# Optimization experiments

Hardware: AMD Instinct MI355X
Metric: run time of the kernel (lower is better)

Reference implementation:

```python
import jax, jax.numpy as jnp
import numpy as np

DEPTH, FEAT, HID = 20, 2048, 1024
HALF = FEAT // 2
CLAMP = 2.0
TWO_OVER_PI = 0.6366197723675814  # FrEIA's 0.636619772


def setup_inputs() -> dict:
    key = jax.random.key(0)
    ks = jax.random.split(key, 9)
    x = jax.random.normal(ks[0], (4096, FEAT), dtype=jnp.float32)
    # FrEIA PermuteRandom: numpy permutation seeded with layer index k
    perms = jnp.asarray(
        np.stack([np.random.RandomState(k).permutation(FEAT) for k in range(DEPTH)]),
        dtype=jnp.int32,
    )
    def w(k, shape):  # module reinits all params as 0.01*randn
        return 0.01 * jax.random.normal(k, shape, dtype=jnp.float32)
    return {
        "x": x, "perms": perms,
        "s1_w1": w(ks[1], (DEPTH, HALF, HID)), "s1_b1": w(ks[2], (DEPTH, HID)),
        "s1_w2": w(ks[3], (DEPTH, HID, FEAT)), "s1_b2": w(ks[4], (DEPTH, FEAT)),
        "s2_w1": w(ks[5], (DEPTH, HALF, HID)), "s2_b1": w(ks[6], (DEPTH, HID)),
        "s2_w2": w(ks[7], (DEPTH, HID, FEAT)), "s2_b2": w(ks[8], (DEPTH, FEAT)),
    }


def _subnet(x, w1, b1, w2, b2):
    h = x @ w1 + b1
    h = jnp.where(h >= 0, h, 0.01 * h)  # LeakyReLU(negative_slope=0.01)
    return h @ w2 + b2


def reference(x, perms, s1_w1, s1_b1, s1_w2, s1_b2, s2_w1, s2_b1, s2_w2, s2_b2):
    def body(carry, xs):
        z, jac = carry
        perm, w1a, b1a, w1b, b1b, w2a, b2a, w2b, b2b = xs
        z = z[:, perm]                       # PermuteRandom
        x1, x2 = z[:, :HALF], z[:, HALF:]    # GLOW coupling split
        r2 = _subnet(x2, w2a, b2a, w2b, b2b)  # [B, FEAT] -> (s2, t2)
        e2 = CLAMP * TWO_OVER_PI * jnp.arctan(r2[:, :HALF] / CLAMP)
        y1 = jnp.exp(e2) * x1 + r2[:, HALF:]
        r1 = _subnet(y1, w1a, b1a, w1b, b1b)  # (s1, t1)
        e1 = CLAMP * TWO_OVER_PI * jnp.arctan(r1[:, :HALF] / CLAMP)
        y2 = jnp.exp(e1) * x2 + r1[:, HALF:]
        jac = jac + e1.sum(-1) + e2.sum(-1)  # log|det J| per sample
        return (jnp.concatenate([y1, y2], axis=-1), jac), None

    jac0 = jnp.zeros(x.shape[0], dtype=x.dtype)
    (z, jac), _ = jax.lax.scan(
        body, (x, jac0),
        (perms, s1_w1, s1_b1, s1_w2, s1_b2, s2_w1, s2_b1, s2_w2, s2_b2),
    )
    return z, jac
```

## Files before the change

### kernel.cpp

```cpp
#include <hip/hip_runtime.h>
#include <stdint.h>

#define DEPTH 20
#define FEAT  2048
#define HALF  1024
#define HID   1024
#define MROWS 4096

typedef __bf16 bf16x8 __attribute__((ext_vector_type(8)));
typedef float  f32x4  __attribute__((ext_vector_type(4)));
typedef unsigned int u32x4 __attribute__((ext_vector_type(4)));

__device__ __forceinline__ unsigned short f2bf(float f) {
  union { float f; unsigned int u; } v; v.f = f;
  unsigned int u = v.u + 0x7fffu + ((v.u >> 16) & 1u);
  return (unsigned short)(u >> 16);
}

__device__ __forceinline__ void async_cp16(unsigned short* lds, const unsigned short* g) {
  __builtin_amdgcn_global_load_lds(
      (const __attribute__((address_space(1))) void*)g,
      (__attribute__((address_space(3))) void*)lds, 16, 0, 0);
}

__device__ __forceinline__ bf16x8 lds_ld8(const unsigned short* p) {
  return __builtin_bit_cast(bf16x8, *(const u32x4*)p);
}

__device__ __forceinline__ void wg_barrier() {
  asm volatile("" ::: "memory");
  __builtin_amdgcn_s_barrier();
  asm volatile("" ::: "memory");
}

__global__ void wcvt_k(const float* __restrict__ s2w1, const float* __restrict__ s2w2,
                       const float* __restrict__ s1w1, const float* __restrict__ s1w2,
                       unsigned short* __restrict__ w2a, unsigned short* __restrict__ w2b,
                       unsigned short* __restrict__ w1a, unsigned short* __restrict__ w1b) {
  const int zid = blockIdx.z;
  const int d = zid >> 2, which = zid & 3;
  const float* src; unsigned short* dst; int N, pp;
  switch (which) {
    case 0:  src = s2w1 + (size_t)d * HALF * HID;  dst = w2a + (size_t)d * HALF * HID; N = 1024; pp = 0; break;
    case 1:  src = s2w2 + (size_t)d * HID * FEAT;  dst = w2b + (size_t)d * FEAT * HID; N = 2048; pp = 1; break;
    case 2:  src = s1w1 + (size_t)d * HALF * HID;  dst = w1a + (size_t)d * HALF * HID; N = 1024; pp = 0; break;
    default: src = s1w2 + (size_t)d * HID * FEAT;  dst = w1b + (size_t)d * FEAT * HID; N = 2048; pp = 1; break;
  }
  int nb = blockIdx.x * 32;
  if (nb >= N) return;
  int kb = blockIdx.y * 32;
  __shared__ float t[32][33];
  int tx = threadIdx.x, ty = threadIdx.y;
#pragma unroll
  for (int s = 0; s < 4; ++s)
    t[ty + 8*s][tx] = src[(size_t)(kb + ty + 8*s) * N + nb + tx];
  __syncthreads();
  int pbase = pp ? (nb < 1024 ? 2*nb : 2*(nb - 1024) + 32) : nb;
#pragma unroll
  for (int s = 0; s < 4; ++s) {
    int nl = ty + 8*s;
    dst[(size_t)(pbase + nl) * 1024 + kb + tx] = f2bf(t[tx][nl]);
  }
}

__device__ __forceinline__ int porig(int p) {
  int g = p >> 6, o = p & 63;
  return (o < 32) ? (g*32 + o) : (1024 + g*32 + (o - 32));
}

__global__ void bias_k(const float* __restrict__ s2b1, const float* __restrict__ s2b2,
                       const float* __restrict__ s1b1, const float* __restrict__ s1b2,
                       float* __restrict__ b2a, float* __restrict__ b2b,
                       float* __restrict__ b1a, float* __restrict__ b1b) {
  int i = blockIdx.x * 256 + threadIdx.x;
  if (i >= DEPTH * 6144) return;
  int d = i / 6144, j = i - d * 6144;
  if (j < 1024)      b2a[d*1024 + j] = s2b1[(size_t)d*HID + j];
  else if (j < 3072) { int p = j - 1024; b2b[d*2048 + p] = s2b2[(size_t)d*FEAT + porig(p)]; }
  else if (j < 4096) b1a[d*1024 + j - 3072] = s1b1[(size_t)d*HID + j - 3072];
  else               { int p = j - 4096; b1b[d*2048 + p] = s1b2[(size_t)d*FEAT + porig(p)]; }
}

__global__ void permute_k(const float* __restrict__ z, const int* __restrict__ perm,
                          float* __restrict__ x1f, float* __restrict__ x2f,
                          unsigned short* __restrict__ x2b) {
  int c = blockIdx.x * 256 + threadIdx.x;
  int row0 = blockIdx.y * 8;
  int pc = perm[c];
#pragma unroll
  for (int r = 0; r < 8; ++r) {
    int row = row0 + r;
    float v = z[row * FEAT + pc];
    if (c < HALF) {
      x1f[row * HALF + c] = v;
    } else {
      x2f[row * HALF + c - HALF] = v;
      x2b[row * HALF + c - HALF] = f2bf(v);
    }
  }
}

template<int EPI>
__launch_bounds__(256)
__global__ void gemm_k(const unsigned short* __restrict__ A,
                       const unsigned short* __restrict__ Bt,
                       const float* __restrict__ bias,
                       const float* __restrict__ xin,
                       float* __restrict__ yout,
                       unsigned short* __restrict__ ybf,
                       float* __restrict__ jac,
                       unsigned short* __restrict__ hout) {
  __shared__ unsigned short As[3][128 * 32];
  __shared__ unsigned short Bs[3][128 * 32];
  const int tid  = threadIdx.x;
  const int wave = tid >> 6, lane = tid & 63;
  const int quad = lane >> 4, l15 = lane & 15;
  const int wy = wave >> 1, wx = wave & 1;
  const int bm = blockIdx.y * 128;
  const int bn = blockIdx.x * 128;
  const int K = 1024;

  f32x4 acc[4][4];
#pragma unroll
  for (int i = 0; i < 4; ++i)
#pragma unroll
    for (int j = 0; j < 4; ++j)
#pragma unroll
      for (int r = 0; r < 4; ++r) acc[i][j][r] = 0.0f;

  const int gbase = wave * 64 + lane;

  auto stage = [&](int kt, int buf) {
    const int k0 = kt * 32;
#pragma unroll
    for (int i = 0; i < 2; ++i) {
      int g  = i * 256 + gbase;
      int r  = g >> 2, kg = g & 3;
      async_cp16(&As[buf][(i * 256 + wave * 64) * 8], A  + (size_t)(bm + r) * K + k0 + kg * 8);
      async_cp16(&Bs[buf][(i * 256 + wave * 64) * 8], Bt + (size_t)(bn + r) * K + k0 + kg * 8);
    }
  };

  stage(0, 0);
  stage(1, 1);

  int cb = 0;
  for (int kt = 0; kt < 32; ++kt) {
    if (kt < 30) {
      stage(kt + 2, (kt + 2) % 3);
      asm volatile("s_waitcnt vmcnt(8)" ::: "memory");
    } else if (kt == 30) {
      asm volatile("s_waitcnt vmcnt(4)" ::: "memory");
    } else {
      asm volatile("s_waitcnt vmcnt(0)" ::: "memory");
    }
    wg_barrier();

    bf16x8 af[4], bf[4];
#pragma unroll
    for (int i = 0; i < 4; ++i)
      af[i] = lds_ld8(&As[cb][(wy * 64 + i * 16 + l15) * 32 + quad * 8]);
#pragma unroll
    for (int j = 0; j < 4; ++j)
      bf[j] = lds_ld8(&Bs[cb][(wx * 64 + j * 16 + l15) * 32 + quad * 8]);
#pragma unroll
    for (int i = 0; i < 4; ++i)
#pragma unroll
      for (int j = 0; j < 4; ++j)
        acc[i][j] = __builtin_amdgcn_mfma_f32_16x16x32_bf16(af[i], bf[j], acc[i][j], 0, 0, 0);

    wg_barrier();
    cb = (cb == 2) ? 0 : cb + 1;
  }

  if (EPI == 0) {
    const int ldo = gridDim.x * 128;
#pragma unroll
    for (int j = 0; j < 4; ++j) {
      int col = bn + wx * 64 + j * 16 + l15;
      float bj = bias[col];
#pragma unroll
      for (int i = 0; i < 4; ++i) {
#pragma unroll
        for (int r = 0; r < 4; ++r) {
          int row = bm + wy * 64 + i * 16 + quad * 4 + r;
          float v = acc[i][j][r] + bj;
          v = v >= 0.0f ? v : 0.01f * v;
          hout[(size_t)row * ldo + col] = f2bf(v);
        }
      }
    }
  } else {
    const int g = (bn >> 6) + wx;
#pragma unroll
    for (int i = 0; i < 4; ++i) {
      float esum[4] = {0.0f, 0.0f, 0.0f, 0.0f};
#pragma unroll
      for (int j = 0; j < 2; ++j) {
        int pe = bn + wx * 64 + j * 16 + l15;
        float be = bias[pe];
        float ba = bias[pe + 32];
        int xcol = g * 32 + j * 16 + l15;
#pragma unroll
        for (int r = 0; r < 4; ++r) {
          int row = bm + wy * 64 + i * 16 + quad * 4 + r;
          float re = acc[i][j][r] + be;
          float ra = acc[i][j + 2][r] + ba;
          float e  = 1.2732395447351628f * atanf(0.5f * re);
          float y  = __expf(e) * xin[(size_t)row * HALF + xcol] + ra;
          yout[(size_t)row * FEAT + xcol] = y;
          if (ybf) ybf[(size_t)row * HALF + xcol] = f2bf(y);
          esum[r] += e;
        }
      }
#pragma unroll
      for (int r = 0; r < 4; ++r) {
        float v = esum[r];
        v += __shfl_xor(v, 1);
        v += __shfl_xor(v, 2);
        v += __shfl_xor(v, 4);
        v += __shfl_xor(v, 8);
        if (l15 == 0) {
          int row = bm + wy * 64 + i * 16 + quad * 4 + r;
          atomicAdd(&jac[row], v);
        }
      }
    }
  }
}

__global__ void jcopy_k(const float* __restrict__ jac, float* __restrict__ out) {
  int i = blockIdx.x * 256 + threadIdx.x;
  if (i < 4096) out[i] = jac[i];
}

extern "C" void kernel_launch(void* const* d_in, const int* in_sizes, int n_in,
                              void* d_out, int out_size, void* d_ws, size_t ws_size,
                              hipStream_t stream) {
  const float* x     = (const float*)d_in[0];
  const int*   perms = (const int*)d_in[1];
  const float* s1w1  = (const float*)d_in[2];
  const float* s1b1  = (const float*)d_in[3];
  const float* s1w2  = (const float*)d_in[4];
  const float* s1b2  = (const float*)d_in[5];
  const float* s2w1  = (const float*)d_in[6];
  const float* s2b1  = (const float*)d_in[7];
  const float* s2w2  = (const float*)d_in[8];
  const float* s2b2  = (const float*)d_in[9];
  float* out = (float*)d_out;

  size_t off = 0;
  char* base = (char*)d_ws;
  auto alloc = [&](size_t bytes) {
    void* r = base + off;
    off += (bytes + 255) & ~(size_t)255;
    return r;
  };
  float*          x1f = (float*)alloc((size_t)MROWS * HALF * 4);
  float*          x2f = (float*)alloc((size_t)MROWS * HALF * 4);
  unsigned short* x2b = (unsigned short*)alloc((size_t)MROWS * HALF * 2);
  unsigned short* y1b = (unsigned short*)alloc((size_t)MROWS * HALF * 2);
  unsigned short* hb  = (unsigned short*)alloc((size_t)MROWS * HID * 2);
  float*          zbuf= (float*)alloc((size_t)MROWS * FEAT * 4);
  unsigned short* w2a = (unsigned short*)alloc((size_t)DEPTH * HALF * HID * 2);
  unsigned short* w2b = (unsigned short*)alloc((size_t)DEPTH * FEAT * HID * 2);
  unsigned short* w1a = (unsigned short*)alloc((size_t)DEPTH * HALF * HID * 2);
  unsigned short* w1b = (unsigned short*)alloc((size_t)DEPTH * FEAT * HID * 2);
  float* b2a = (float*)alloc((size_t)DEPTH * 1024 * 4);
  float* b2b = (float*)alloc((size_t)DEPTH * 2048 * 4);
  float* b1a = (float*)alloc((size_t)DEPTH * 1024 * 4);
  float* b1b = (float*)alloc((size_t)DEPTH * 2048 * 4);
  float* jac = (float*)alloc(4096 * 4);

  hipMemsetAsync(jac, 0, 4096 * 4, stream);

  wcvt_k<<<dim3(64, 32, 4 * DEPTH), dim3(32, 8), 0, stream>>>(
      s2w1, s2w2, s1w1, s1w2, w2a, w2b, w1a, w1b);
  bias_k<<<(DEPTH * 6144 + 255) / 256, 256, 0, stream>>>(
      s2b1, s2b2, s1b1, s1b2, b2a, b2b, b1a, b1b);

  for (int d = 0; d < DEPTH; ++d) {
    const float* zsrc = (d == 0) ? x : zbuf;
    permute_k<<<dim3(8, 512), 256, 0, stream>>>(zsrc, perms + (size_t)d * FEAT, x1f, x2f, x2b);

    unsigned short* W2a = w2a + (size_t)d * HALF * HID;
    unsigned short* W2b = w2b + (size_t)d * FEAT * HID;
    unsigned short* W1a = w1a + (size_t)d * HALF * HID;
    unsigned short* W1b = w1b + (size_t)d * FEAT * HID;
    float* B2a = b2a + (size_t)d * 1024;
    float* B2b = b2b + (size_t)d * 2048;
    float* B1a = b1a + (size_t)d * 1024;
    float* B1b = b1b + (size_t)d * 2048;

    float* zdst = (d == DEPTH - 1) ? out : zbuf;
    gemm_k<0><<<dim3(8, 32), 256, 0, stream>>>(x2b, W2a, B2a, nullptr, nullptr, nullptr, nullptr, hb);
    gemm_k<1><<<dim3(16, 32), 256, 0, stream>>>(hb, W2b, B2b, x1f, zdst, y1b, jac, nullptr);
    gemm_k<0><<<dim3(8, 32), 256, 0, stream>>>(y1b, W1a, B1a, nullptr, nullptr, nullptr, nullptr, hb);
    gemm_k<1><<<dim3(16, 32), 256, 0, stream>>>(hb, W1b, B1b, x2f, zdst + HALF, nullptr, jac, nullptr);
  }
  jcopy_k<<<16, 256, 0, stream>>>(jac, out + (size_t)MROWS * FEAT);
}
```

Before: 4.081 ms.

## Fuse next-layer permutation into coupling epilogue and simplify GEMM pipeline

Precomputes inverse permutations and has the coupling GEMM epilogue scatter outputs directly into the next layer's permuted x1/x2/bf16 buffers (ping-ponged), eliminating the per-layer permute kernel and the z round trip. The GEMM loses its triple-buffered async prefetch in favor of a single buffer with full waits, and the hidden-layer GEMMs use 64-row tiles for more blocks. The weight conversion kernel processes taller tiles with paired bf16 stores. Scattered epilogue writes are less coalesced, and the unpipelined main loop exposes memory latency.

```diff
diff --git a/kernel.cpp b/kernel.cpp
--- a/kernel.cpp
+++ b/kernel.cpp
@@ -25,12 +25,6 @@
 
 __device__ __forceinline__ bf16x8 lds_ld8(const unsigned short* p) {
   return __builtin_bit_cast(bf16x8, *(const u32x4*)p);
-}
-
-__device__ __forceinline__ void wg_barrier() {
-  asm volatile("" ::: "memory");
-  __builtin_amdgcn_s_barrier();
-  asm volatile("" ::: "memory");
 }
 
 __global__ void wcvt_k(const float* __restrict__ s2w1, const float* __restrict__ s2w2,
@@ -48,18 +42,21 @@
   }
   int nb = blockIdx.x * 32;
   if (nb >= N) return;
-  int kb = blockIdx.y * 32;
-  __shared__ float t[32][33];
+  int kb = blockIdx.y * 64;
+  __shared__ float t[64][33];
   int tx = threadIdx.x, ty = threadIdx.y;
 #pragma unroll
-  for (int s = 0; s < 4; ++s)
+  for (int s = 0; s < 8; ++s)
     t[ty + 8*s][tx] = src[(size_t)(kb + ty + 8*s) * N + nb + tx];
   __syncthreads();
   int pbase = pp ? (nb < 1024 ? 2*nb : 2*(nb - 1024) + 32) : nb;
 #pragma unroll
   for (int s = 0; s < 4; ++s) {
     int nl = ty + 8*s;
-    dst[(size_t)(pbase + nl) * 1024 + kb + tx] = f2bf(t[tx][nl]);
+    ushort2 w;
+    w.x = f2bf(t[2*tx][nl]);
+    w.y = f2bf(t[2*tx + 1][nl]);
+    *(ushort2*)&dst[(size_t)(pbase + nl) * 1024 + kb + 2*tx] = w;
   }
 }
 
@@ -81,6 +78,13 @@
   else               { int p = j - 4096; b1b[d*2048 + p] = s1b2[(size_t)d*FEAT + porig(p)]; }
 }
 
+__global__ void invp_k(const int* __restrict__ perms, int* __restrict__ invp) {
+  int i = blockIdx.x * 256 + threadIdx.x;
+  if (i >= DEPTH * FEAT) return;
+  int d = i >> 11, c = i & 2047;
+  invp[(d << 11) | perms[i]] = c;
+}
+
 __global__ void permute_k(const float* __restrict__ z, const int* __restrict__ perm,
                           float* __restrict__ x1f, float* __restrict__ x2f,
                           unsigned short* __restrict__ x2b) {
@@ -106,23 +110,31 @@
                        const unsigned short* __restrict__ Bt,
                        const float* __restrict__ bias,
                        const float* __restrict__ xin,
-                       float* __restrict__ yout,
+                       const int* __restrict__ invp,
+                       float* __restrict__ nx1,
+                       float* __restrict__ nx2,
+                       unsigned short* __restrict__ nx2b,
+                       float* __restrict__ outz,
+                       int zbase,
                        unsigned short* __restrict__ ybf,
                        float* __restrict__ jac,
                        unsigned short* __restrict__ hout) {
-  __shared__ unsigned short As[3][128 * 32];
-  __shared__ unsigned short Bs[3][128 * 32];
+  constexpr int BM = EPI ? 128 : 64;
+  constexpr int MI = EPI ? 4 : 2;
+  constexpr int WR = EPI ? 64 : 32;
+  __shared__ unsigned short As[BM * 32];
+  __shared__ unsigned short Bs[128 * 32];
   const int tid  = threadIdx.x;
   const int wave = tid >> 6, lane = tid & 63;
   const int quad = lane >> 4, l15 = lane & 15;
   const int wy = wave >> 1, wx = wave & 1;
-  const int bm = blockIdx.y * 128;
+  const int bm = blockIdx.y * BM;
   const int bn = blockIdx.x * 128;
   const int K = 1024;
 
-  f32x4 acc[4][4];
-#pragma unroll
-  for (int i = 0; i < 4; ++i)
+  f32x4 acc[MI][4];
+#pragma unroll
+  for (int i = 0; i < MI; ++i)
 #pragma unroll
     for (int j = 0; j < 4; ++j)
 #pragma unroll
@@ -130,47 +142,36 @@
 
   const int gbase = wave * 64 + lane;
 
-  auto stage = [&](int kt, int buf) {
+  for (int kt = 0; kt < 32; ++kt) {
     const int k0 = kt * 32;
+#pragma unroll
+    for (int i = 0; i < BM / 64; ++i) {
+      int g  = i * 256 + gbase;
+      int r  = g >> 2, kg = g & 3;
+      async_cp16(&As[(i * 256 + wave * 64) * 8], A  + (size_t)(bm + r) * K + k0 + kg * 8);
+    }
 #pragma unroll
     for (int i = 0; i < 2; ++i) {
       int g  = i * 256 + gbase;
       int r  = g >> 2, kg = g & 3;
-      async_cp16(&As[buf][(i * 256 + wave * 64) * 8], A  + (size_t)(bm + r) * K + k0 + kg * 8);
-      async_cp16(&Bs[buf][(i * 256 + wave * 64) * 8], Bt + (size_t)(bn + r) * K + k0 + kg * 8);
-    }
-  };
-
-  stage(0, 0);
-  stage(1, 1);
-
-  int cb = 0;
-  for (int kt = 0; kt < 32; ++kt) {
-    if (kt < 30) {
-      stage(kt + 2, (kt + 2) % 3);
-      asm volatile("s_waitcnt vmcnt(8)" ::: "memory");
-    } else if (kt == 30) {
-      asm volatile("s_waitcnt vmcnt(4)" ::: "memory");
-    } else {
-      asm volatile("s_waitcnt vmcnt(0)" ::: "memory");
-    }
-    wg_barrier();
-
-    bf16x8 af[4], bf[4];
-#pragma unroll
-    for (int i = 0; i < 4; ++i)
-      af[i] = lds_ld8(&As[cb][(wy * 64 + i * 16 + l15) * 32 + quad * 8]);
+      async_cp16(&Bs[(i * 256 + wave * 64) * 8], Bt + (size_t)(bn + r) * K + k0 + kg * 8);
+    }
+    asm volatile("s_waitcnt vmcnt(0)" ::: "memory");
+    __syncthreads();
+
+    bf16x8 af[MI], bf[4];
+#pragma unroll
+    for (int i = 0; i < MI; ++i)
+      af[i] = lds_ld8(&As[(wy * WR + i * 16 + l15) * 32 + quad * 8]);
 #pragma unroll
     for (int j = 0; j < 4; ++j)
-      bf[j] = lds_ld8(&Bs[cb][(wx * 64 + j * 16 + l15) * 32 + quad * 8]);
-#pragma unroll
-    for (int i = 0; i < 4; ++i)
+      bf[j] = lds_ld8(&Bs[(wx * 64 + j * 16 + l15) * 32 + quad * 8]);
+#pragma unroll
+    for (int i = 0; i < MI; ++i)
 #pragma unroll
       for (int j = 0; j < 4; ++j)
         acc[i][j] = __builtin_amdgcn_mfma_f32_16x16x32_bf16(af[i], bf[j], acc[i][j], 0, 0, 0);
-
-    wg_barrier();
-    cb = (cb == 2) ? 0 : cb + 1;
+    __syncthreads();
   }
 
   if (EPI == 0) {
@@ -180,10 +181,10 @@
       int col = bn + wx * 64 + j * 16 + l15;
       float bj = bias[col];
 #pragma unroll
-      for (int i = 0; i < 4; ++i) {
+      for (int i = 0; i < MI; ++i) {
 #pragma unroll
         for (int r = 0; r < 4; ++r) {
-          int row = bm + wy * 64 + i * 16 + quad * 4 + r;
+          int row = bm + wy * WR + i * 16 + quad * 4 + r;
           float v = acc[i][j][r] + bj;
           v = v >= 0.0f ? v : 0.01f * v;
           hout[(size_t)row * ldo + col] = f2bf(v);
@@ -192,24 +193,38 @@
     }
   } else {
     const int g = (bn >> 6) + wx;
+    float be[2], ba[2];
+    int xcol[2], route[2];
+#pragma unroll
+    for (int j = 0; j < 2; ++j) {
+      int pe = bn + wx * 64 + j * 16 + l15;
+      be[j] = bias[pe];
+      ba[j] = bias[pe + 32];
+      xcol[j] = g * 32 + j * 16 + l15;
+      int zcol = zbase + xcol[j];
+      route[j] = invp ? invp[zcol] : zcol;
+    }
 #pragma unroll
     for (int i = 0; i < 4; ++i) {
       float esum[4] = {0.0f, 0.0f, 0.0f, 0.0f};
 #pragma unroll
       for (int j = 0; j < 2; ++j) {
-        int pe = bn + wx * 64 + j * 16 + l15;
-        float be = bias[pe];
-        float ba = bias[pe + 32];
-        int xcol = g * 32 + j * 16 + l15;
 #pragma unroll
         for (int r = 0; r < 4; ++r) {
           int row = bm + wy * 64 + i * 16 + quad * 4 + r;
-          float re = acc[i][j][r] + be;
-          float ra = acc[i][j + 2][r] + ba;
+          float re = acc[i][j][r] + be[j];
+          float ra = acc[i][j + 2][r] + ba[j];
           float e  = 1.2732395447351628f * atanf(0.5f * re);
-          float y  = __expf(e) * xin[(size_t)row * HALF + xcol] + ra;
-          yout[(size_t)row * FEAT + xcol] = y;
-          if (ybf) ybf[(size_t)row * HALF + xcol] = f2bf(y);
+          float y  = __expf(e) * xin[(size_t)row * HALF + xcol[j]] + ra;
+          if (!invp) {
+            outz[(size_t)row * FEAT + route[j]] = y;
+          } else if (route[j] < HALF) {
+            nx1[(size_t)row * HALF + route[j]] = y;
+          } else {
+            nx2[(size_t)row * HALF + route[j] - HALF] = y;
+            nx2b[(size_t)row * HALF + route[j] - HALF] = f2bf(y);
+          }
+          if (ybf) ybf[(size_t)row * HALF + xcol[j]] = f2bf(y);
           esum[r] += e;
         }
       }
@@ -256,12 +271,15 @@
     off += (bytes + 255) & ~(size_t)255;
     return r;
   };
-  float*          x1f = (float*)alloc((size_t)MROWS * HALF * 4);
-  float*          x2f = (float*)alloc((size_t)MROWS * HALF * 4);
-  unsigned short* x2b = (unsigned short*)alloc((size_t)MROWS * HALF * 2);
+  float*          x1f[2]; float* x2f[2]; unsigned short* x2b[2];
+  x1f[0] = (float*)alloc((size_t)MROWS * HALF * 4);
+  x1f[1] = (float*)alloc((size_t)MROWS * HALF * 4);
+  x2f[0] = (float*)alloc((size_t)MROWS * HALF * 4);
+  x2f[1] = (float*)alloc((size_t)MROWS * HALF * 4);
+  x2b[0] = (unsigned short*)alloc((size_t)MROWS * HALF * 2);
+  x2b[1] = (unsigned short*)alloc((size_t)MROWS * HALF * 2);
   unsigned short* y1b = (unsigned short*)alloc((size_t)MROWS * HALF * 2);
   unsigned short* hb  = (unsigned short*)alloc((size_t)MROWS * HID * 2);
-  float*          zbuf= (float*)alloc((size_t)MROWS * FEAT * 4);
   unsigned short* w2a = (unsigned short*)alloc((size_t)DEPTH * HALF * HID * 2);
   unsigned short* w2b = (unsigned short*)alloc((size_t)DEPTH * FEAT * HID * 2);
   unsigned short* w1a = (unsigned short*)alloc((size_t)DEPTH * HALF * HID * 2);
@@ -270,18 +288,23 @@
   float* b2b = (float*)alloc((size_t)DEPTH * 2048 * 4);
   float* b1a = (float*)alloc((size_t)DEPTH * 1024 * 4);
   float* b1b = (float*)alloc((size_t)DEPTH * 2048 * 4);
+  int*   invp = (int*)alloc((size_t)DEPTH * FEAT * 4);
   float* jac = (float*)alloc(4096 * 4);
 
   hipMemsetAsync(jac, 0, 4096 * 4, stream);
 
-  wcvt_k<<<dim3(64, 32, 4 * DEPTH), dim3(32, 8), 0, stream>>>(
+  wcvt_k<<<dim3(64, 16, 4 * DEPTH), dim3(32, 8), 0, stream>>>(
       s2w1, s2w2, s1w1, s1w2, w2a, w2b, w1a, w1b);
   bias_k<<<(DEPTH * 6144 + 255) / 256, 256, 0, stream>>>(
       s2b1, s2b2, s1b1, s1b2, b2a, b2b, b1a, b1b);
+  invp_k<<<(DEPTH * FEAT + 255) / 256, 256, 0, stream>>>(perms, invp);
+
+  permute_k<<<dim3(8, 512), 256, 0, stream>>>(x, perms, x1f[0], x2f[0], x2b[0]);
 
   for (int d = 0; d < DEPTH; ++d) {
-    const float* zsrc = (d == 0) ? x : zbuf;
-    permute_k<<<dim3(8, 512), 256, 0, stream>>>(zsrc, perms + (size_t)d * FEAT, x1f, x2f, x2b);
+    const int par = d & 1, nxt = par ^ 1;
+    const bool last = (d == DEPTH - 1);
+    const int* ip = last ? nullptr : invp + (size_t)(d + 1) * FEAT;
 
     unsigned short* W2a = w2a + (size_t)d * HALF * HID;
     unsigned short* W2b = w2b + (size_t)d * FEAT * HID;
@@ -292,11 +315,14 @@
     float* B1a = b1a + (size_t)d * 1024;
     float* B1b = b1b + (size_t)d * 2048;
 
-    float* zdst = (d == DEPTH - 1) ? out : zbuf;
-    gemm_k<0><<<dim3(8, 32), 256, 0, stream>>>(x2b, W2a, B2a, nullptr, nullptr, nullptr, nullptr, hb);
-    gemm_k<1><<<dim3(16, 32), 256, 0, stream>>>(hb, W2b, B2b, x1f, zdst, y1b, jac, nullptr);
-    gemm_k<0><<<dim3(8, 32), 256, 0, stream>>>(y1b, W1a, B1a, nullptr, nullptr, nullptr, nullptr, hb);
-    gemm_k<1><<<dim3(16, 32), 256, 0, stream>>>(hb, W1b, B1b, x2f, zdst + HALF, nullptr, jac, nullptr);
+    gemm_k<0><<<dim3(8, 64), 256, 0, stream>>>(
+        x2b[par], W2a, B2a, nullptr, nullptr, nullptr, nullptr, nullptr, nullptr, 0, nullptr, nullptr, hb);
+    gemm_k<1><<<dim3(16, 32), 256, 0, stream>>>(
+        hb, W2b, B2b, x1f[par], ip, x1f[nxt], x2f[nxt], x2b[nxt], out, 0, y1b, jac, nullptr);
+    gemm_k<0><<<dim3(8, 64), 256, 0, stream>>>(
+        y1b, W1a, B1a, nullptr, nullptr, nullptr, nullptr, nullptr, nullptr, 0, nullptr, nullptr, hb);
+    gemm_k<1><<<dim3(16, 32), 256, 0, stream>>>(
+        hb, W1b, B1b, x2f[par], ip, x1f[nxt], x2f[nxt], x2b[nxt], out, HALF, nullptr, jac, nullptr);
   }
   jcopy_k<<<16, 256, 0, stream>>>(jac, out + (size_t)MROWS * FEAT);
 }
```

New measurement: 5.243 ms. 1.28x slower.
